# Optimization experiments

Hardware: AMD Instinct MI355X
Metric: run time of the kernel (lower is better)

## Reference

```python
import jax, jax.numpy as jnp
import numpy as np


def setup_inputs() -> dict:
    key = jax.random.key(0)
    k1, k2, k3 = jax.random.split(key, 3)
    B, C, H, D, N = 4, 2048, 8, 512, 1024
    std = 1.0 / np.sqrt(D)
    query = jax.random.normal(k1, (B, C, H, D), dtype=jnp.float32)
    keyl = jax.random.uniform(k2, (H, N, D // 2), minval=-std, maxval=std, dtype=jnp.float32)
    keyr = jax.random.uniform(k3, (H, N, D // 2), minval=-std, maxval=std, dtype=jnp.float32)
    return {"query": query, "keyl": keyl, "keyr": keyr, "num_subkeys": N, "top_k": 32}


def reference(query, keyl, keyr, num_subkeys, top_k):
    # query: [B, C, H, D]; keys: [H, N, D//2]
    sub = query.shape[-1] // 2
    ql, qr = query[..., :sub], query[..., sub:]
    scorel = jnp.einsum('bcnq,nkq->bcnk', ql, keyl)  # [B,C,H,N]
    scorer = jnp.einsum('bcnq,nkq->bcnk', qr, keyr)
    top_keys_l, top_idx_l = jax.lax.top_k(scorel, top_k)  # [B,C,H,k]
    top_keys_r, top_idx_r = jax.lax.top_k(scorer, top_k)
    # product grid of scores: [B,C,H,k,k] -> [B,C,H,k*k]
    product_scores = (top_keys_l[..., :, None] + top_keys_r[..., None, :])
    product_scores = product_scores.reshape(*product_scores.shape[:-2], top_k * top_k)
    # NOTE: faithful to the source, which expands BOTH index tensors along the
    # last (column) axis (a quirk/bug: indices_r is not transposed like scores_r).
    flat_idx = top_idx_l * num_subkeys + top_idx_r  # [B,C,H,k]
    product_indices = jnp.broadcast_to(flat_idx[..., :, None],
                                       (*flat_idx.shape, top_k))
    product_indices = product_indices.reshape(*product_scores.shape)
    top_product_scores, top_product_indices = jax.lax.top_k(product_scores, top_k)
    selected_value_weights = jax.nn.softmax(top_product_scores, axis=-1)
    selected_value_indices = jnp.take_along_axis(product_indices, top_product_indices, axis=-1)
    return selected_value_weights, selected_value_indices
```

## Files before the change

### kernel.cpp

```cpp
#include <hip/hip_runtime.h>
#include <math.h>

#define Hh  8
#define Dd  512
#define SUB 256
#define Nk  1024
#define TK  32
#define Rr  8
#define NT  256
#define W_ELEMS (65536 * 32)


__device__ __forceinline__ float wave_fmax_bcast(float x) {
    int v;
    v = __builtin_amdgcn_update_dpp(0xff800000, __float_as_int(x), 0x111, 0xf, 0xf, false);
    x = fmaxf(x, __int_as_float(v));
    v = __builtin_amdgcn_update_dpp(0xff800000, __float_as_int(x), 0x112, 0xf, 0xf, false);
    x = fmaxf(x, __int_as_float(v));
    v = __builtin_amdgcn_update_dpp(0xff800000, __float_as_int(x), 0x114, 0xf, 0xf, false);
    x = fmaxf(x, __int_as_float(v));
    v = __builtin_amdgcn_update_dpp(0xff800000, __float_as_int(x), 0x118, 0xf, 0xf, false);
    x = fmaxf(x, __int_as_float(v));
    v = __builtin_amdgcn_update_dpp(0xff800000, __float_as_int(x), 0x142, 0xa, 0xf, false);
    x = fmaxf(x, __int_as_float(v));
    v = __builtin_amdgcn_update_dpp(0xff800000, __float_as_int(x), 0x143, 0xc, 0xf, false);
    x = fmaxf(x, __int_as_float(v));
    return __int_as_float(__builtin_amdgcn_readlane(__float_as_int(x), 63));
}

__global__ __launch_bounds__(NT, 2)
void pk_kernel(const float* __restrict__ query,
               const float* __restrict__ keyl,
               const float* __restrict__ keyr,
               float* __restrict__ out)
{
    __shared__ __attribute__((aligned(16))) float qs[Rr][Dd];
    __shared__ __attribute__((aligned(16))) float sc[4][Nk];
    __shared__ __attribute__((aligned(16))) float topv[2][Rr][TK];
    __shared__ __attribute__((aligned(16))) int   topi[2][Rr][TK];

    const int bid  = blockIdx.x;
    const int h    = bid >> 10;
    const int tile = bid & 1023;
    const int bc0  = tile * Rr;
    const int t    = threadIdx.x;
    const int lane = t & 63;
    const int wave = t >> 6;

    #pragma unroll
    for (int rw = 0; rw < 2; ++rw) {
        const int r = wave * 2 + rw;
        const float4* src = (const float4*)(query + ((size_t)(bc0 + r) * Hh + h) * Dd);
        float4* dst = (float4*)qs[r];
        dst[lane]      = src[lane];
        dst[lane + 64] = src[lane + 64];
    }
    __syncthreads();

    const int X = ((t >> 4) & 7) << 2;

    for (int side = 0; side < 2; ++side) {
        const float* kbase = (side == 0 ? keyl : keyr) + (size_t)h * Nk * SUB;

        const float4* kr0 = (const float4*)(kbase + (size_t)(0 * 256 + t) * SUB);
        const float4* kr1 = (const float4*)(kbase + (size_t)(1 * 256 + t) * SUB);
        const float4* kr2 = (const float4*)(kbase + (size_t)(2 * 256 + t) * SUB);
        const float4* kr3 = (const float4*)(kbase + (size_t)(3 * 256 + t) * SUB);

        float acc[Rr][4];
        #pragma unroll
        for (int r = 0; r < Rr; ++r)
            #pragma unroll
            for (int g = 0; g < 4; ++g) acc[r][g] = 0.0f;

        #pragma unroll 1
        for (int js = 0; js < 16; ++js) {
            #pragma unroll
            for (int c = 0; c < 4; ++c) {
                const int idx = 4 * js + c;
                float4 k0 = kr0[idx], k1 = kr1[idx], k2 = kr2[idx], k3 = kr3[idx];
                #pragma unroll
                for (int r = 0; r < Rr; ++r) {
                    float4 qv = ((const float4*)&qs[r][side * SUB])[idx];
                    acc[r][0] = fmaf(qv.x, k0.x, acc[r][0]);
                    acc[r][1] = fmaf(qv.x, k1.x, acc[r][1]);
                    acc[r][2] = fmaf(qv.x, k2.x, acc[r][2]);
                    acc[r][3] = fmaf(qv.x, k3.x, acc[r][3]);
                    acc[r][0] = fmaf(qv.y, k0.y, acc[r][0]);
                    acc[r][1] = fmaf(qv.y, k1.y, acc[r][1]);
                    acc[r][2] = fmaf(qv.y, k2.y, acc[r][2]);
                    acc[r][3] = fmaf(qv.y, k3.y, acc[r][3]);
                    acc[r][0] = fmaf(qv.z, k0.z, acc[r][0]);
                    acc[r][1] = fmaf(qv.z, k1.z, acc[r][1]);
                    acc[r][2] = fmaf(qv.z, k2.z, acc[r][2]);
                    acc[r][3] = fmaf(qv.z, k3.z, acc[r][3]);
                    acc[r][0] = fmaf(qv.w, k0.w, acc[r][0]);
                    acc[r][1] = fmaf(qv.w, k1.w, acc[r][1]);
                    acc[r][2] = fmaf(qv.w, k2.w, acc[r][2]);
                    acc[r][3] = fmaf(qv.w, k3.w, acc[r][3]);
                }
            }
        }

        #pragma unroll
        for (int batch = 0; batch < 2; ++batch) {
            #pragma unroll
            for (int rr = 0; rr < 4; ++rr)
                #pragma unroll
                for (int g = 0; g < 4; ++g)
                    sc[rr][g * 256 + (t ^ X)] = acc[batch * 4 + rr][g];
            __syncthreads();

            const int r = batch * 4 + wave;
            float v[16];
            const float4* sp = (const float4*)sc[wave];
            #pragma unroll
            for (int c = 0; c < 4; ++c) {
                const int gidx = (4 * lane + c) ^ (lane & 7);
                float4 x = sp[gidx];
                v[4*c+0] = x.x; v[4*c+1] = x.y; v[4*c+2] = x.z; v[4*c+3] = x.w;
            }
            for (int it = 0; it < TK; ++it) {
                float lv = v[0]; int li = 0;
                #pragma unroll
                for (int i = 1; i < 16; ++i)
                    if (v[i] > lv) { lv = v[i]; li = i; }
                float M = wave_fmax_bcast(lv);
                const int w = (int)__builtin_ctzll(__ballot(lv == M));
                if (lane == w) { topv[side][r][it] = M; topi[side][r][it] = (lane << 4) | li; }
                const bool kk = (lane == w);
                #pragma unroll
                for (int i = 0; i < 16; ++i)
                    v[i] = (kk && i == li) ? -INFINITY : v[i];
            }
            __syncthreads();
        }
    }

    {
        const int ra = wave, rb = wave + 4;
        float va[16], vb[16];
        const float tla = topv[0][ra][lane >> 1];
        const float tlb = topv[0][rb][lane >> 1];
        const float4* t1a = (const float4*)topv[1][ra];
        const float4* t1b = (const float4*)topv[1][rb];
        #pragma unroll
        for (int c = 0; c < 4; ++c) {
            float4 xa = t1a[4 * (lane & 1) + c];
            float4 xb = t1b[4 * (lane & 1) + c];
            va[4*c+0] = __fadd_rn(tla, xa.x); va[4*c+1] = __fadd_rn(tla, xa.y);
            va[4*c+2] = __fadd_rn(tla, xa.z); va[4*c+3] = __fadd_rn(tla, xa.w);
            vb[4*c+0] = __fadd_rn(tlb, xb.x); vb[4*c+1] = __fadd_rn(tlb, xb.y);
            vb[4*c+2] = __fadd_rn(tlb, xb.z); vb[4*c+3] = __fadd_rn(tlb, xb.w);
        }
        float m0a = 0.0f, wva = 0.0f; int wpa = 0;
        float m0b = 0.0f, wvb = 0.0f; int wpb = 0;
        for (int it = 0; it < TK; ++it) {
            float la = va[0]; int ia = 0;
            float lb = vb[0]; int ib = 0;
            #pragma unroll
            for (int i = 1; i < 16; ++i) {
                if (va[i] > la) { la = va[i]; ia = i; }
                if (vb[i] > lb) { lb = vb[i]; ib = i; }
            }
            float Ma = wave_fmax_bcast(la);
            float Mb = wave_fmax_bcast(lb);
            const int wa = (int)__builtin_ctzll(__ballot(la == Ma));
            const int wb = (int)__builtin_ctzll(__ballot(lb == Mb));
            const int pa = (wa << 4) | __builtin_amdgcn_readlane(ia, wa);
            const int pb = (wb << 4) | __builtin_amdgcn_readlane(ib, wb);
            if (it == 0) { m0a = Ma; m0b = Mb; }
            if (lane == it) { wva = Ma; wpa = pa; wvb = Mb; wpb = pb; }
            const bool ka = (lane == wa), kb = (lane == wb);
            #pragma unroll
            for (int i = 0; i < 16; ++i) {
                va[i] = (ka && i == ia) ? -INFINITY : va[i];
                vb[i] = (kb && i == ib) ? -INFINITY : vb[i];
            }
        }
        float ea = (lane < TK) ? expf(wva - m0a) : 0.0f;
        float eb = (lane < TK) ? expf(wvb - m0b) : 0.0f;
        float sa = ea, sb = eb;
        #pragma unroll
        for (int m = 1; m < 64; m <<= 1) {
            sa += __shfl_xor(sa, m, 64);
            sb += __shfl_xor(sb, m, 64);
        }
        if (lane < TK) {
            {
                const int bc = bc0 + ra;
                const size_t base = ((size_t)bc * Hh + h) * TK;
                const int a = wpa >> 5;
                const int fl = topi[0][ra][a] * Nk + topi[1][ra][a];
                out[base + lane] = ea / sa;
                out[(size_t)W_ELEMS + base + lane] = (float)fl;
            }
            {
                const int bc = bc0 + rb;
                const size_t base = ((size_t)bc * Hh + h) * TK;
                const int a = wpb >> 5;
                const int fl = topi[0][rb][a] * Nk + topi[1][rb][a];
                out[base + lane] = eb / sb;
                out[(size_t)W_ELEMS + base + lane] = (float)fl;
            }
        }
    }
}

extern "C" void kernel_launch(void* const* d_in, const int* in_sizes, int n_in,
                              void* d_out, int out_size, void* d_ws, size_t ws_size,
                              hipStream_t stream)
{
    const float* query = (const float*)d_in[0];
    const float* keyl  = (const float*)d_in[1];
    const float* keyr  = (const float*)d_in[2];
    float* out = (float*)d_out;
    pk_kernel<<<dim3(8192), dim3(NT), 0, stream>>>(query, keyl, keyr, out);
}
```

Measured before the change: 2.497 ms.

## Prefetch key vectors one step ahead, tree argmax, per-side query staging

The dot-product loop is flattened to 64 steps and loads the next float4 of each of the four key rows while the current one is being consumed, so global load latency overlaps the FMAs. The serial 16-element argmax scan becomes a pairwise tree, which shortens the dependency chain in every top-k iteration. The query tile is now staged in shared memory one half at a time, which halves its LDS footprint at the cost of an extra barrier per side. Tie-breaking in the tree argmax still prefers the lower index, but this needs checking for exact equality with the earlier scan.

Result: slower. 4.168 ms (+66.9%).

```diff
diff --git a/kernel.cpp b/kernel.cpp
--- a/kernel.cpp
+++ b/kernel.cpp
@@ -28,13 +28,40 @@
     return __int_as_float(__builtin_amdgcn_readlane(__float_as_int(x), 63));
 }
 
+__device__ __forceinline__ void argmax16(const float v[16], float& lv, int& li) {
+    float w1[8]; int j1[8];
+    #pragma unroll
+    for (int i = 0; i < 8; ++i) {
+        const bool g = v[2*i+1] > v[2*i];
+        w1[i] = g ? v[2*i+1] : v[2*i];
+        j1[i] = g ? 2*i+1 : 2*i;
+    }
+    float w2[4]; int j2[4];
+    #pragma unroll
+    for (int i = 0; i < 4; ++i) {
+        const bool g = w1[2*i+1] > w1[2*i];
+        w2[i] = g ? w1[2*i+1] : w1[2*i];
+        j2[i] = g ? j1[2*i+1] : j1[2*i];
+    }
+    float w3[2]; int j3[2];
+    #pragma unroll
+    for (int i = 0; i < 2; ++i) {
+        const bool g = w2[2*i+1] > w2[2*i];
+        w3[i] = g ? w2[2*i+1] : w2[2*i];
+        j3[i] = g ? j2[2*i+1] : j2[2*i];
+    }
+    const bool g = w3[1] > w3[0];
+    lv = g ? w3[1] : w3[0];
+    li = g ? j3[1] : j3[0];
+}
+
 __global__ __launch_bounds__(NT, 2)
 void pk_kernel(const float* __restrict__ query,
                const float* __restrict__ keyl,
                const float* __restrict__ keyr,
                float* __restrict__ out)
 {
-    __shared__ __attribute__((aligned(16))) float qs[Rr][Dd];
+    __shared__ __attribute__((aligned(16))) float qs[Rr][SUB];
     __shared__ __attribute__((aligned(16))) float sc[4][Nk];
     __shared__ __attribute__((aligned(16))) float topv[2][Rr][TK];
     __shared__ __attribute__((aligned(16))) int   topi[2][Rr][TK];
@@ -47,21 +74,21 @@
     const int lane = t & 63;
     const int wave = t >> 6;
 
-    #pragma unroll
-    for (int rw = 0; rw < 2; ++rw) {
-        const int r = wave * 2 + rw;
-        const float4* src = (const float4*)(query + ((size_t)(bc0 + r) * Hh + h) * Dd);
-        float4* dst = (float4*)qs[r];
-        dst[lane]      = src[lane];
-        dst[lane + 64] = src[lane + 64];
-    }
-    __syncthreads();
-
     const int X = ((t >> 4) & 7) << 2;
 
     for (int side = 0; side < 2; ++side) {
+        {
+            const int r0 = wave * 2;
+            const float4* s0 = (const float4*)(query +
+                ((size_t)(bc0 + r0) * Hh + h) * Dd + side * SUB);
+            const float4* s1 = (const float4*)(query +
+                ((size_t)(bc0 + r0 + 1) * Hh + h) * Dd + side * SUB);
+            ((float4*)qs[r0])[lane]     = s0[lane];
+            ((float4*)qs[r0 + 1])[lane] = s1[lane];
+        }
+        __syncthreads();
+
         const float* kbase = (side == 0 ? keyl : keyr) + (size_t)h * Nk * SUB;
-
         const float4* kr0 = (const float4*)(kbase + (size_t)(0 * 256 + t) * SUB);
         const float4* kr1 = (const float4*)(kbase + (size_t)(1 * 256 + t) * SUB);
         const float4* kr2 = (const float4*)(kbase + (size_t)(2 * 256 + t) * SUB);
@@ -73,33 +100,32 @@
             #pragma unroll
             for (int g = 0; g < 4; ++g) acc[r][g] = 0.0f;
 
+        float4 kc0 = kr0[0], kc1 = kr1[0], kc2 = kr2[0], kc3 = kr3[0];
         #pragma unroll 1
-        for (int js = 0; js < 16; ++js) {
-            #pragma unroll
-            for (int c = 0; c < 4; ++c) {
-                const int idx = 4 * js + c;
-                float4 k0 = kr0[idx], k1 = kr1[idx], k2 = kr2[idx], k3 = kr3[idx];
-                #pragma unroll
-                for (int r = 0; r < Rr; ++r) {
-                    float4 qv = ((const float4*)&qs[r][side * SUB])[idx];
-                    acc[r][0] = fmaf(qv.x, k0.x, acc[r][0]);
-                    acc[r][1] = fmaf(qv.x, k1.x, acc[r][1]);
-                    acc[r][2] = fmaf(qv.x, k2.x, acc[r][2]);
-                    acc[r][3] = fmaf(qv.x, k3.x, acc[r][3]);
-                    acc[r][0] = fmaf(qv.y, k0.y, acc[r][0]);
-                    acc[r][1] = fmaf(qv.y, k1.y, acc[r][1]);
-                    acc[r][2] = fmaf(qv.y, k2.y, acc[r][2]);
-                    acc[r][3] = fmaf(qv.y, k3.y, acc[r][3]);
-                    acc[r][0] = fmaf(qv.z, k0.z, acc[r][0]);
-                    acc[r][1] = fmaf(qv.z, k1.z, acc[r][1]);
-                    acc[r][2] = fmaf(qv.z, k2.z, acc[r][2]);
-                    acc[r][3] = fmaf(qv.z, k3.z, acc[r][3]);
-                    acc[r][0] = fmaf(qv.w, k0.w, acc[r][0]);
-                    acc[r][1] = fmaf(qv.w, k1.w, acc[r][1]);
-                    acc[r][2] = fmaf(qv.w, k2.w, acc[r][2]);
-                    acc[r][3] = fmaf(qv.w, k3.w, acc[r][3]);
-                }
-            }
+        for (int idx = 0; idx < 64; ++idx) {
+            const int nx = (idx + 1) & 63;
+            float4 kn0 = kr0[nx], kn1 = kr1[nx], kn2 = kr2[nx], kn3 = kr3[nx];
+            #pragma unroll
+            for (int r = 0; r < Rr; ++r) {
+                float4 qv = ((const float4*)qs[r])[idx];
+                acc[r][0] = fmaf(qv.x, kc0.x, acc[r][0]);
+                acc[r][1] = fmaf(qv.x, kc1.x, acc[r][1]);
+                acc[r][2] = fmaf(qv.x, kc2.x, acc[r][2]);
+                acc[r][3] = fmaf(qv.x, kc3.x, acc[r][3]);
+                acc[r][0] = fmaf(qv.y, kc0.y, acc[r][0]);
+                acc[r][1] = fmaf(qv.y, kc1.y, acc[r][1]);
+                acc[r][2] = fmaf(qv.y, kc2.y, acc[r][2]);
+                acc[r][3] = fmaf(qv.y, kc3.y, acc[r][3]);
+                acc[r][0] = fmaf(qv.z, kc0.z, acc[r][0]);
+                acc[r][1] = fmaf(qv.z, kc1.z, acc[r][1]);
+                acc[r][2] = fmaf(qv.z, kc2.z, acc[r][2]);
+                acc[r][3] = fmaf(qv.z, kc3.z, acc[r][3]);
+                acc[r][0] = fmaf(qv.w, kc0.w, acc[r][0]);
+                acc[r][1] = fmaf(qv.w, kc1.w, acc[r][1]);
+                acc[r][2] = fmaf(qv.w, kc2.w, acc[r][2]);
+                acc[r][3] = fmaf(qv.w, kc3.w, acc[r][3]);
+            }
+            kc0 = kn0; kc1 = kn1; kc2 = kn2; kc3 = kn3;
         }
 
         #pragma unroll
@@ -121,10 +147,8 @@
                 v[4*c+0] = x.x; v[4*c+1] = x.y; v[4*c+2] = x.z; v[4*c+3] = x.w;
             }
             for (int it = 0; it < TK; ++it) {
-                float lv = v[0]; int li = 0;
-                #pragma unroll
-                for (int i = 1; i < 16; ++i)
-                    if (v[i] > lv) { lv = v[i]; li = i; }
+                float lv; int li;
+                argmax16(v, lv, li);
                 float M = wave_fmax_bcast(lv);
                 const int w = (int)__builtin_ctzll(__ballot(lv == M));
                 if (lane == w) { topv[side][r][it] = M; topi[side][r][it] = (lane << 4) | li; }
@@ -156,26 +180,22 @@
         float m0a = 0.0f, wva = 0.0f; int wpa = 0;
         float m0b = 0.0f, wvb = 0.0f; int wpb = 0;
         for (int it = 0; it < TK; ++it) {
-            float la = va[0]; int ia = 0;
-            float lb = vb[0]; int ib = 0;
-            #pragma unroll
-            for (int i = 1; i < 16; ++i) {
-                if (va[i] > la) { la = va[i]; ia = i; }
-                if (vb[i] > lb) { lb = vb[i]; ib = i; }
-            }
+            float la, lb; int ia_, ib_;
+            argmax16(va, la, ia_);
+            argmax16(vb, lb, ib_);
             float Ma = wave_fmax_bcast(la);
             float Mb = wave_fmax_bcast(lb);
             const int wa = (int)__builtin_ctzll(__ballot(la == Ma));
             const int wb = (int)__builtin_ctzll(__ballot(lb == Mb));
-            const int pa = (wa << 4) | __builtin_amdgcn_readlane(ia, wa);
-            const int pb = (wb << 4) | __builtin_amdgcn_readlane(ib, wb);
+            const int pa = (wa << 4) | __builtin_amdgcn_readlane(ia_, wa);
+            const int pb = (wb << 4) | __builtin_amdgcn_readlane(ib_, wb);
             if (it == 0) { m0a = Ma; m0b = Mb; }
             if (lane == it) { wva = Ma; wpa = pa; wvb = Mb; wpb = pb; }
             const bool ka = (lane == wa), kb = (lane == wb);
             #pragma unroll
             for (int i = 0; i < 16; ++i) {
-                va[i] = (ka && i == ia) ? -INFINITY : va[i];
-                vb[i] = (kb && i == ib) ? -INFINITY : vb[i];
+                va[i] = (ka && i == ia_) ? -INFINITY : va[i];
+                vb[i] = (kb && i == ib_) ? -INFINITY : vb[i];
             }
         }
         float ea = (lane < TK) ? expf(wva - m0a) : 0.0f;
```
